# Kernel tuning notes

Measured on AMD Instinct MI355X. Metric: run time of the kernel, lower is better.

## Reference

```python
import jax, jax.numpy as jnp
import numpy as np

B, T, LMAX = 8, 4000, 2048
VOCAB, D, H = 20000, 128, 128
SCALE = float(H) ** 0.5  # torch uses pow(hidden_dim, 0.5) with hidden_dim=128 even though feature dim is 256


def setup_inputs() -> dict:
    key = jax.random.key(0)
    ks = jax.random.split(key, 22)
    def n(k, sh, s=0.05):
        return jax.random.normal(k, sh, dtype=jnp.float32) * s
    token_ids = jax.random.randint(ks[0], (B, T), 0, VOCAB)
    lens = jax.random.randint(ks[1], (B,), LMAX // 4, LMAX).at[0].set(LMAX)
    return dict(
        token_ids=token_ids, lens=lens,
        embed=n(ks[2], (VOCAB, D)),
        gru_wih0=n(ks[3], (2, 3 * H, D)), gru_whh0=n(ks[4], (2, 3 * H, H)),
        gru_bih0=n(ks[5], (2, 3 * H)), gru_bhh0=n(ks[6], (2, 3 * H)),
        gru_wih1=n(ks[7], (2, 3 * H, 2 * H)), gru_whh1=n(ks[8], (2, 3 * H, H)),
        gru_bih1=n(ks[9], (2, 3 * H)), gru_bhh1=n(ks[10], (2, 3 * H)),
        conv_w=n(ks[11], (3, D, D, 2)), conv_b=n(ks[12], (3, D)),
        Wa_w=n(ks[13], (2 * H, 4 * H)), Wa_b=n(ks[14], (2 * H,)),
        VT_w=n(ks[15], (1, 2 * H)), VT_b=n(ks[16], (1,)),
        Qw=n(ks[17], (2 * H, 2 * H)), Kw=n(ks[18], (2 * H, 2 * H)), Vw=n(ks[19], (2 * H, 2 * H)),
        fc_w=n(ks[20], (6, 2 * H)), fc_b=n(ks[21], (6,)),
    )


def _gru_dir(x, mask, Wih, Whh, bih, bhh):
    # One direction of a torch GRU layer with packed-sequence semantics:
    # outputs are zero past each sample's length; state frozen there.
    xg = jnp.einsum('bld,gd->blg', x, Wih) + bih   # [B, L, 3H] precomputed input gates
    xg = jnp.swapaxes(xg, 0, 1)                    # [L, B, 3H]
    m = jnp.swapaxes(mask, 0, 1)                   # [L, B]
    h0 = jnp.zeros((x.shape[0], H), x.dtype)

    def step(h, inp):
        g, mt = inp
        hh = h @ Whh.T + bhh
        r = jax.nn.sigmoid(g[:, :H] + hh[:, :H])
        z = jax.nn.sigmoid(g[:, H:2 * H] + hh[:, H:2 * H])
        nn_ = jnp.tanh(g[:, 2 * H:] + r * hh[:, 2 * H:])
        hn = (1.0 - z) * nn_ + z * h
        h2 = jnp.where(mt[:, None] > 0, hn, h)
        return h2, hn * mt[:, None]

    _, out = jax.lax.scan(step, h0, (xg, m))
    return jnp.swapaxes(out, 0, 1)                 # [B, L, H]


def _bi_gru_layer(x, mask, rev_idx, wih, whh, bih, bhh):
    out_f = _gru_dir(x, mask, wih[0], whh[0], bih[0], bhh[0])
    # packed bi-GRU: backward direction runs over each sample's reversed VALID segment
    xr = jnp.take_along_axis(x, rev_idx[:, :, None], axis=1)
    out_b = _gru_dir(xr, mask, wih[1], whh[1], bih[1], bhh[1])
    out_b = jnp.take_along_axis(out_b, rev_idx[:, :, None], axis=1) * mask[:, :, None]
    return jnp.concatenate([out_f, out_b], axis=-1)


def _additive_attn(s, enc, mask, Wa_w, Wa_b, VT_w, VT_b):
    sb = jnp.broadcast_to(s, enc.shape)
    x = jnp.concatenate([sb, enc], axis=-1)                     # [B, L, 4H]
    sh = jnp.tanh(jnp.einsum('blk,hk->blh', x, Wa_w) + Wa_b)
    res = jnp.einsum('blh,oh->blo', sh, VT_w)[..., 0] + VT_b[0]  # [B, L]
    # torch multiplies scores by 0/1 mask BEFORE softmax (pads get score 0, not -inf)
    w = jax.nn.softmax(res * mask, axis=-1)
    return jnp.sum(enc * w[..., None], axis=1, keepdims=True)   # [B, 1, 2H]


def _forward(embed, gru_wih0, gru_whh0, gru_bih0, gru_bhh0, gru_wih1, gru_whh1, gru_bih1, gru_bhh1,
             conv_w, conv_b, Wa_w, Wa_b, VT_w, VT_b, Qw, Kw, Vw, fc_w, fc_b, token_ids, lens):
    emb = embed[token_ids]                                      # [B, T, D]
    tpos = jnp.arange(LMAX)
    mask = (tpos[None, :] < lens[:, None]).astype(emb.dtype)    # [B, LMAX]
    rev_idx = jnp.where(tpos[None, :] < lens[:, None], lens[:, None] - 1 - tpos[None, :], tpos[None, :])
    pad_data = emb[:, :LMAX] * mask[..., None]                  # pad_packed_sequence zeroes pads

    # conv backbone runs on the FULL 4000-length padded embedding (as in torch), then trimmed/masked
    x = jnp.swapaxes(emb, 1, 2)                                 # [B, D, T]
    for i in range(3):
        x = jax.lax.conv_general_dilated(x, conv_w[i], (1,), 'VALID',
                                         dimension_numbers=('NCH', 'OIH', 'NCH'))
        x = jax.nn.relu(x + conv_b[i][None, :, None])
    conv_out = jnp.swapaxes(x, 1, 2)[:, :LMAX] * mask[..., None]  # [B, LMAX, D]

    h1 = _bi_gru_layer(pad_data, mask, rev_idx, gru_wih0, gru_whh0, gru_bih0, gru_bhh0)
    enc = _bi_gru_layer(h1, mask, rev_idx, gru_wih1, gru_whh1, gru_bih1, gru_bhh1)  # [B, LMAX, 2H]

    tmean = jnp.mean(conv_out, axis=1)                          # mean over padded length, as torch
    s = jnp.repeat(tmean, 2, axis=-1)[:, None, :]               # expand+reshape => interleaved duplicate [B,1,2H]

    inp2 = jnp.concatenate([pad_data, pad_data], axis=-1)       # [B, LMAX, 2H]
    Q = inp2 @ Qw.T
    K = inp2 @ Kw.T
    V = inp2 @ Vw.T
    scores = jnp.einsum('bqd,bkd->bqk', Q, K) / SCALE
    W = jax.nn.softmax(scores, axis=0)                          # torch F.softmax implicit dim -> 0 for 3D input
    W = W * mask[:, :, None]                                    # mask broadcast over key axis (query rows masked)
    Z = jnp.einsum('bqk,bkd->bqd', W, V)
    sa = jnp.sum(Z, axis=1, keepdims=True)                      # [B, 1, 2H]

    d1 = _additive_attn(s, enc, mask, Wa_w, Wa_b, VT_w, VT_b)
    d2 = _additive_attn(sa, enc, mask, Wa_w, Wa_b, VT_w, VT_b)
    dinput = 0.5 * (d1 + d2)                                    # mean over the concat dim
    return dinput @ fc_w.T + fc_b                               # [B, 1, 6]


def reference(token_ids, lens, embed, gru_wih0, gru_whh0, gru_bih0, gru_bhh0, gru_wih1, gru_whh1,
              gru_bih1, gru_bhh1, conv_w, conv_b, Wa_w, Wa_b, VT_w, VT_b, Qw, Kw, Vw, fc_w, fc_b):
    return _forward(embed, gru_wih0, gru_whh0, gru_bih0, gru_bhh0, gru_wih1, gru_whh1, gru_bih1,
                    gru_bhh1, conv_w, conv_b, Wa_w, Wa_b, VT_w, VT_b, Qw, Kw, Vw, fc_w, fc_b,
                    token_ids, lens)
```

## Files before the change

### kernel.cpp

```cpp
#include <hip/hip_runtime.h>
#include <stdint.h>

typedef unsigned short u16;
typedef unsigned int u32;
typedef __attribute__((ext_vector_type(8))) short short8;
typedef __attribute__((ext_vector_type(8))) u16 u16x8;
typedef __attribute__((ext_vector_type(4))) float f32x4;
typedef __attribute__((ext_vector_type(2))) float f32x2;
typedef __attribute__((ext_vector_type(2))) u32 u32x2;

#define DEVINL static __device__ __forceinline__

#if !__has_builtin(__builtin_amdgcn_exp2f)
#define __builtin_amdgcn_exp2f(x) exp2f(x)
#endif
#if !__has_builtin(__builtin_amdgcn_rcpf)
#define __builtin_amdgcn_rcpf(x) (1.0f/(x))
#endif

#define MFMA16(a, b, c) __builtin_amdgcn_mfma_f32_16x16x32_bf16((a), (b), (c), 0, 0, 0)

constexpr float LOG2E_C    = 1.4426950408889634f;
constexpr float TWOLOG2E_C = 2.8853900817779268f;
constexpr float RSCALE_LG  = 1.4426950408889634f / 11.313708498984761f;

constexpr size_t A256(size_t x){ return (x + 255) & ~(size_t)255; }
constexpr size_t OFS_EMB   = 0;
constexpr size_t OFS_PAD   = A256(OFS_EMB  + (size_t)8*2051*128*2);
constexpr size_t OFS_X1    = A256(OFS_PAD  + (size_t)8*2048*128*2);
constexpr size_t OFS_X2    = A256(OFS_X1   + (size_t)8*2050*128*2);
constexpr size_t OFS_QKVW  = A256(OFS_X2   + (size_t)8*2049*128*2);
constexpr size_t OFS_WA2   = A256(OFS_QKVW + (size_t)3*256*128*2);
constexpr size_t OFS_CONVW = A256(OFS_WA2  + (size_t)256*256*2);
constexpr size_t OFS_WIH0  = A256(OFS_CONVW+ (size_t)3*128*256*2);
constexpr size_t OFS_WIH1  = A256(OFS_WIH0 + (size_t)2*384*128*2);
constexpr size_t OFS_BIASX = A256(OFS_WIH1 + (size_t)2*384*256*2);
constexpr size_t OFS_BHHN  = A256(OFS_BIASX+ (size_t)2*2*384*4);
constexpr size_t OFS_Q     = A256(OFS_BHHN + (size_t)2*2*128*4);
constexpr size_t OFS_K     = A256(OFS_Q    + (size_t)8*2048*256*2);
constexpr size_t OFS_V     = A256(OFS_K    + (size_t)8*2048*256*2);
constexpr size_t OFS_CS    = A256(OFS_V    + (size_t)8*2048*256*2);
constexpr size_t OFS_TM    = A256(OFS_CS   + (size_t)8*2048*4);
constexpr size_t OFS_XG    = A256(OFS_TM   + (size_t)8*128*4);
constexpr size_t OFS_H1    = A256(OFS_XG   + (size_t)2*2048*8*384*4);
constexpr size_t OFS_ENC   = A256(OFS_H1   + (size_t)8*2048*256*2);
constexpr size_t OFS_ENCW  = A256(OFS_ENC  + (size_t)8*2048*256*2);
constexpr size_t OFS_SA    = A256(OFS_ENCW + (size_t)8*2048*256*4);
constexpr size_t OFS_RES   = A256(OFS_SA   + (size_t)8*256*4);
constexpr size_t OFS_DV    = A256(OFS_RES  + (size_t)8*2*2048*4);

DEVINL u16 f2bf(float f){
  u32 u = __builtin_bit_cast(u32, f);
  u32 r = (u + 0x7FFFu + ((u >> 16) & 1u)) >> 16;
  return (u16)r;
}
DEVINL float bf2f(u16 s){ return __builtin_bit_cast(float, (u32)s << 16); }

DEVINL short8 ld8cvt(const float* p, float sc){
  short8 o;
#pragma unroll
  for (int e = 0; e < 8; ++e) o[e] = (short)f2bf(p[e]*sc);
  return o;
}

DEVINL u32 cvtpk(float lo, float hi){
  u32 r;
  asm("v_cvt_pk_bf16_f32 %0, %1, %2" : "=v"(r) : "v"(lo), "v"(hi));
  return r;
}

DEVINL float sel4(const f32x4 v, int rr){
  float a = (rr & 1) ? v[1] : v[0];
  float bq = (rr & 1) ? v[3] : v[2];
  return (rr & 2) ? bq : a;
}

__global__ __launch_bounds__(256) void k_prep(
    const int* tok, const int* lens, const float* embed,
    const float* wih0, const float* wih1,
    const float* bih0, const float* bhh0, const float* bih1, const float* bhh1,
    const float* convw, const float* WaW, const float* Qw, const float* Kw, const float* Vw,
    char* ws)
{
  u16* emb_bf   = (u16*)(ws + OFS_EMB);
  u16* pad_bf   = (u16*)(ws + OFS_PAD);
  u16* qkvw     = (u16*)(ws + OFS_QKVW);
  u16* wa2      = (u16*)(ws + OFS_WA2);
  u16* convw_bf = (u16*)(ws + OFS_CONVW);
  u16* wih0_bf  = (u16*)(ws + OFS_WIH0);
  u16* wih1_bf  = (u16*)(ws + OFS_WIH1);
  float* biasx  = (float*)(ws + OFS_BIASX);
  float* bhhn   = (float*)(ws + OFS_BHHN);
  float* colsum = (float*)(ws + OFS_CS);
  float* tmean  = (float*)(ws + OFS_TM);
  const int S0 = 8*2051*128, S1 = 8*2048*128, S2 = 3*256*128, S3 = 256*256, S4 = 3*128*256;
  const int S5 = 2*384*128, S6 = 2*384*256, S7 = 2*2*384 + 2*2*128, S8 = 8*2048 + 8*128;
  const int TOT = S0+S1+S2+S3+S4+S5+S6+S7+S8;
  for (int i = blockIdx.x*256 + threadIdx.x; i < TOT; i += gridDim.x*256){
    int j = i;
    if (j < S0){
      int b = j / (2051*128); int r = j - b*(2051*128); int t = r >> 7, dd = r & 127;
      emb_bf[j] = f2bf(embed[(size_t)tok[b*4000 + t]*128 + dd]);
      continue;
    }
    j -= S0;
    if (j < S1){
      int b = j >> 18; int r = j & 262143; int t = r >> 7, dd = r & 127;
      float v = (t < lens[b]) ? embed[(size_t)tok[b*4000 + t]*128 + dd] : 0.f;
      pad_bf[j] = f2bf(v); continue;
    }
    j -= S1;
    if (j < S2){
      int z = j >> 15; int r = j & 32767; int o = r >> 7, k2 = r & 127;
      const float* W = (z == 0) ? Qw : (z == 1) ? Kw : Vw;
      qkvw[j] = f2bf(W[o*256 + k2] + W[o*256 + 128 + k2]); continue;
    }
    j -= S2;
    if (j < S3){ int h = j >> 8, k2 = j & 255; wa2[j] = f2bf(WaW[(size_t)h*512 + 256 + k2]); continue; }
    j -= S3;
    if (j < S4){
      int ly = j >> 15; int r = j & 32767; int o = r >> 8, k2 = r & 255;
      int i2 = k2 & 127, kap = k2 >> 7;
      convw_bf[j] = f2bf(convw[((size_t)(ly*128 + o)*128 + i2)*2 + kap]); continue;
    }
    j -= S4;
    if (j < S5){ wih0_bf[j] = f2bf(wih0[j]); continue; }
    j -= S5;
    if (j < S6){ wih1_bf[j] = f2bf(wih1[j]); continue; }
    j -= S6;
    if (j < S7){
      if (j < 1536){
        int ly = j / 768; int r = j - ly*768; int d = r / 384, g = r % 384;
        float bi = (ly ? bih1 : bih0)[d*384 + g];
        float bh = (ly ? bhh1 : bhh0)[d*384 + g];
        biasx[j] = (g < 256) ? (-LOG2E_C*(bi + bh)) : (TWOLOG2E_C*bi);
      } else {
        int j2 = j - 1536; int ly = j2 >> 8; int r = j2 & 255; int d = r >> 7, jj = r & 127;
        bhhn[j2] = TWOLOG2E_C*((ly ? bhh1 : bhh0)[d*384 + 256 + jj]);
      }
      continue;
    }
    j -= S7;
    if (j < 8*2048) colsum[j] = 0.f; else tmean[j - 8*2048] = 0.f;
  }
}

template<int LIN, int LOUT, int LAYER>
__global__ __launch_bounds__(256, 1) void k_conv(const int* lens, const float* convb, char* ws){
  const int tt = blockIdx.x, b = blockIdx.y;
  const u16* in = (LAYER == 0) ? (const u16*)(ws + OFS_EMB)
                : (LAYER == 1) ? (const u16*)(ws + OFS_X1) : (const u16*)(ws + OFS_X2);
  u16* out = (LAYER == 0) ? (u16*)(ws + OFS_X1) : (u16*)(ws + OFS_X2);
  const u16* wmat = (const u16*)(ws + OFS_CONVW) + (size_t)LAYER*128*256;
  float* tmean = (float*)(ws + OFS_TM);
  __shared__ __align__(16) u16 sA[65][136];
  const int tid = threadIdx.x, w = tid >> 6, l = tid & 63, rowg = l >> 4, cl = l & 15;
  for (int idx = tid; idx < 65*16; idx += 256){
    int row = idx >> 4, chn = idx & 15;
    int t = tt*64 + row;
    u16x8 v = {0,0,0,0,0,0,0,0};
    if (t < LIN) v = *(const u16x8*)(in + ((size_t)(b*LIN + t))*128 + chn*8);
    *(u16x8*)&sA[row][chn*8] = v;
  }
  __syncthreads();
  f32x4 acc[8];
#pragma unroll
  for (int nt = 0; nt < 8; ++nt) acc[nt] = f32x4{0.f,0.f,0.f,0.f};
#pragma unroll
  for (int kk = 0; kk < 8; ++kk){
    const int rofs = (kk >= 4) ? 1 : 0;
    short8 a = *(const short8*)&sA[w*16 + cl + rofs][(kk & 3)*32 + rowg*8];
#pragma unroll
    for (int nt = 0; nt < 8; ++nt){
      short8 bb = *(const short8*)(wmat + (size_t)(nt*16 + cl)*256 + kk*32 + rowg*8);
      acc[nt] = MFMA16(a, bb, acc[nt]);
    }
  }
  if (LAYER < 2){
#pragma unroll
    for (int nt = 0; nt < 8; ++nt){
      int o = nt*16 + cl;
      float bias = convb[LAYER*128 + o];
#pragma unroll
      for (int r = 0; r < 4; ++r){
        int t = tt*64 + w*16 + rowg*4 + r;
        if (t < LOUT) out[((size_t)(b*LOUT + t))*128 + o] = f2bf(fmaxf(acc[nt][r] + bias, 0.f));
      }
    }
  } else {
    const int lenb = lens[b];
#pragma unroll
    for (int nt = 0; nt < 8; ++nt){
      int o = nt*16 + cl;
      float bias = convb[2*128 + o];
      float s = 0.f;
#pragma unroll
      for (int r = 0; r < 4; ++r){
        int t = tt*64 + w*16 + rowg*4 + r;
        if (t < lenb) s += fmaxf(acc[nt][r] + bias, 0.f);
      }
      s += __shfl_xor(s, 16); s += __shfl_xor(s, 32);
      if (l < 16) atomicAdd(&tmean[b*128 + o], s);
    }
  }
}

__global__ __launch_bounds__(256, 1) void k_qkv(char* ws){
  const int tt = blockIdx.x, b = blockIdx.y, z = blockIdx.z;
  const u16* in = (const u16*)(ws + OFS_PAD);
  const u16* wmat = (const u16*)(ws + OFS_QKVW) + (size_t)z*256*128;
  u16* out = (u16*)(ws + ((z == 0) ? OFS_Q : (z == 1) ? OFS_K : OFS_V));
  __shared__ __align__(16) u16 sA[64][136];
  const int tid = threadIdx.x, w = tid >> 6, l = tid & 63, rowg = l >> 4, cl = l & 15;
  for (int idx = tid; idx < 64*16; idx += 256){
    int row = idx >> 4, chn = idx & 15;
    int t = tt*64 + row;
    *(u16x8*)&sA[row][chn*8] = *(const u16x8*)(in + ((size_t)(b*2048 + t))*128 + chn*8);
  }
  __syncthreads();
  f32x4 acc[16];
#pragma unroll
  for (int nt = 0; nt < 16; ++nt) acc[nt] = f32x4{0.f,0.f,0.f,0.f};
#pragma unroll
  for (int kk = 0; kk < 4; ++kk){
    short8 a = *(const short8*)&sA[w*16 + cl][kk*32 + rowg*8];
#pragma unroll
    for (int nt = 0; nt < 16; ++nt){
      short8 bb = *(const short8*)(wmat + (size_t)(nt*16 + cl)*128 + kk*32 + rowg*8);
      acc[nt] = MFMA16(a, bb, acc[nt]);
    }
  }
#pragma unroll
  for (int nt = 0; nt < 16; ++nt){
    int o = nt*16 + cl;
#pragma unroll
    for (int r = 0; r < 4; ++r){
      int t = tt*64 + w*16 + rowg*4 + r;
      out[((size_t)(b*2048 + t))*256 + o] = f2bf(acc[nt][r]);
    }
  }
}

__global__ __launch_bounds__(256, 1) void k_scores(const int* lens, char* ws){
  const int kt = blockIdx.x, qt = blockIdx.y;
  const u16* Qp = (const u16*)(ws + OFS_Q);
  const u16* Kp = (const u16*)(ws + OFS_K);
  float* colsum = (float*)(ws + OFS_CS);
  __shared__ __align__(16) u16 sQ[64][264];
  __shared__ __align__(16) u16 sK[64][264];
  __shared__ float cbuf[8][64];
  const int tid = threadIdx.x, w = tid >> 6, l = tid & 63, rowg = l >> 4, cl = l & 15;
  for (int i = tid; i < 512; i += 256) cbuf[i >> 6][i & 63] = 0.f;
  f32x4 c[8][4];
#pragma unroll
  for (int b = 0; b < 8; ++b)
#pragma unroll
    for (int nt = 0; nt < 4; ++nt) c[b][nt] = f32x4{0.f,0.f,0.f,0.f};
#pragma unroll
  for (int b = 0; b < 8; ++b){
    __syncthreads();
    for (int idx = tid; idx < 4096; idx += 256){
      int which = idx >> 11, row = (idx >> 5) & 63, ch = idx & 31;
      if (which){
        *(u16x8*)&sK[row][ch*8] = *(const u16x8*)(Kp + ((size_t)(b*2048 + kt*64 + row))*256 + ch*8);
      } else {
        *(u16x8*)&sQ[row][ch*8] = *(const u16x8*)(Qp + ((size_t)(b*2048 + qt*64 + row))*256 + ch*8);
      }
    }
    __syncthreads();
#pragma unroll
    for (int kk = 0; kk < 8; ++kk){
      short8 a = *(const short8*)&sQ[w*16 + cl][kk*32 + rowg*8];
#pragma unroll
      for (int nt = 0; nt < 4; ++nt){
        short8 bb = *(const short8*)&sK[nt*16 + cl][kk*32 + rowg*8];
        c[b][nt] = MFMA16(a, bb, c[b][nt]);
      }
    }
  }
  int lenv[8];
#pragma unroll
  for (int b = 0; b < 8; ++b) lenv[b] = lens[b];
  const int q0 = qt*64 + w*16 + rowg*4;
  float cs[8][4];
#pragma unroll
  for (int b = 0; b < 8; ++b)
#pragma unroll
    for (int nt = 0; nt < 4; ++nt) cs[b][nt] = 0.f;
#pragma unroll
  for (int nt = 0; nt < 4; ++nt){
#pragma unroll
    for (int r = 0; r < 4; ++r){
      float m = c[0][nt][r];
#pragma unroll
      for (int b = 1; b < 8; ++b) m = fmaxf(m, c[b][nt][r]);
      float e[8], s = 0.f;
#pragma unroll
      for (int b = 0; b < 8; ++b){ e[b] = __builtin_amdgcn_exp2f((c[b][nt][r] - m)*RSCALE_LG); s += e[b]; }
      float ri = __builtin_amdgcn_rcpf(s);
#pragma unroll
      for (int b = 0; b < 8; ++b)
        if (q0 + r < lenv[b]) cs[b][nt] += e[b]*ri;
    }
  }
#pragma unroll
  for (int b = 0; b < 8; ++b)
#pragma unroll
    for (int nt = 0; nt < 4; ++nt){
      float v = cs[b][nt];
      v += __shfl_xor(v, 16); v += __shfl_xor(v, 32);
      if (l < 16) atomicAdd(&cbuf[b][nt*16 + l], v);
    }
  __syncthreads();
  for (int i = tid; i < 512; i += 256)
    atomicAdd(&colsum[(size_t)(i >> 6)*2048 + kt*64 + (i & 63)], cbuf[i >> 6][i & 63]);
}

template<int KIN>
__global__ __launch_bounds__(256, 1) void k_xg(const int* lens, char* ws){
  const int tt = blockIdx.x, b = blockIdx.y, dir = blockIdx.z;
  constexpr int LAYER = (KIN == 128) ? 0 : 1;
  const u16* in = (KIN == 128) ? (const u16*)(ws + OFS_PAD) : (const u16*)(ws + OFS_H1);
  const u16* wmat = ((KIN == 128) ? (const u16*)(ws + OFS_WIH0) : (const u16*)(ws + OFS_WIH1))
                    + (size_t)dir*384*KIN;
  const float* biasx = (const float*)(ws + OFS_BIASX) + (LAYER*2 + dir)*384;
  float* xg = (float*)(ws + OFS_XG) + (size_t)dir*2048*3072;
  const int lenb = lens[b];
  __shared__ __align__(16) u16 sA[64][KIN + 8];
  constexpr int CH = KIN/8;
  const int tid = threadIdx.x, w = tid >> 6, l = tid & 63, rowg = l >> 4, cl = l & 15;
  for (int idx = tid; idx < 64*CH; idx += 256){
    int row = idx / CH, chn = idx % CH;
    int t = tt*64 + row;
    int tr = dir ? ((t < lenb) ? (lenb - 1 - t) : t) : t;
    *(u16x8*)&sA[row][chn*8] = *(const u16x8*)(in + ((size_t)(b*2048 + tr))*KIN + chn*8);
  }
  __syncthreads();
  f32x4 acc[24];
#pragma unroll
  for (int nt = 0; nt < 24; ++nt) acc[nt] = f32x4{0.f,0.f,0.f,0.f};
#pragma unroll
  for (int kk = 0; kk < KIN/32; ++kk){
    short8 a = *(const short8*)&sA[w*16 + cl][kk*32 + rowg*8];
#pragma unroll
    for (int nt = 0; nt < 24; ++nt){
      short8 bb = *(const short8*)(wmat + (size_t)(nt*16 + cl)*KIN + kk*32 + rowg*8);
      acc[nt] = MFMA16(a, bb, acc[nt]);
    }
  }
#pragma unroll
  for (int nt = 0; nt < 24; ++nt){
    const int g = nt*16 + cl;
    const float bx = biasx[g];
    const float sc = (nt < 16) ? -LOG2E_C : TWOLOG2E_C;
#pragma unroll
    for (int r = 0; r < 4; ++r){
      const int t = tt*64 + w*16 + rowg*4 + r;
      xg[((size_t)t*8 + b)*384 + g] = sc*acc[nt][r] + bx;
    }
  }
}

__global__ __launch_bounds__(512, 1) void k_rec(const float* xg_all, const float* whh_all,
    const float* bhhn_all, const int* lens, u16* out)
{
  const int dir = blockIdx.x >> 3;
  const int b   = blockIdx.x & 7;
  const float* xg  = xg_all + (size_t)dir*2048*3072 + b*384;
  const float* whh = whh_all + (size_t)dir*384*128;
  const float* bnd = bhhn_all + dir*128;
  const int tid = threadIdx.x;
  const int u = tid >> 6, l = tid & 63;
  const int c = l & 15, q = l >> 4;
  const int rsel = c & 3;
  const int j = u*16 + q*4 + rsel;
  const bool writer = (c < 4);
  const bool dirb = (dir != 0);
  const int lenb = lens[b];

  __shared__ __align__(16) u16 hbuf[2][128];
  if (tid < 256) (&hbuf[0][0])[tid] = 0;

  short8 aR[4], aZ[4], aN[4];
#pragma unroll
  for (int kk = 0; kk < 4; ++kk){
    int k0 = kk*32 + q*8;
    int row = u*16 + c;
    aR[kk] = ld8cvt(whh + (size_t)(row)*128 + k0, -LOG2E_C);
    aZ[kk] = ld8cvt(whh + (size_t)(128 + row)*128 + k0, -LOG2E_C);
    aN[kk] = ld8cvt(whh + (size_t)(256 + row)*128 + k0, TWOLOG2E_C);
  }
  f32x4 bnU;
#pragma unroll
  for (int r = 0; r < 4; ++r) bnU[r] = bnd[u*16 + q*4 + r];

  const int offR = u*16 + q*4;
  const int offXN = 256 + j;
  u16* outp = out + (size_t)b*2048*256 + dir*128 + j;
  float hp = 0.f;

#define LOAD_STAGE(T_, Rv, Zv, Xn) do {              \
    const float* pb_ = xg + (size_t)(T_)*3072;       \
    Rv = *(const f32x4*)(pb_ + offR);                \
    Zv = *(const f32x4*)(pb_ + offR + 128);          \
    Xn = pb_[offXN];                                 \
  } while (0)

#define REC_STEP(T_, PF_, CUR_, Rv, Zv, Xn) do {                                      \
    short8 bf0_ = *(const short8*)(&hbuf[CUR_][0] + (q*8 + 0*32));                    \
    short8 bf1_ = *(const short8*)(&hbuf[CUR_][0] + (q*8 + 1*32));                    \
    short8 bf2_ = *(const short8*)(&hbuf[CUR_][0] + (q*8 + 2*32));                    \
    short8 bf3_ = *(const short8*)(&hbuf[CUR_][0] + (q*8 + 3*32));                    \
    f32x4 cR_ = MFMA16(aR[0], bf0_, Rv);                                              \
    f32x4 cZ_ = MFMA16(aZ[0], bf0_, Zv);                                              \
    f32x4 cN_ = MFMA16(aN[0], bf0_, bnU);                                             \
    const float* pfb_ = xg + (size_t)(PF_)*3072;                                      \
    Rv = *(const f32x4*)(pfb_ + offR);                                                \
    Zv = *(const f32x4*)(pfb_ + offR + 128);                                          \
    float Xnew_ = pfb_[offXN];                                                        \
    cR_ = MFMA16(aR[1], bf1_, cR_);                                                   \
    cZ_ = MFMA16(aZ[1], bf1_, cZ_);                                                   \
    cN_ = MFMA16(aN[1], bf1_, cN_);                                                   \
    cR_ = MFMA16(aR[2], bf2_, cR_);                                                   \
    cZ_ = MFMA16(aZ[2], bf2_, cZ_);                                                   \
    cN_ = MFMA16(aN[2], bf2_, cN_);                                                   \
    cR_ = MFMA16(aR[3], bf3_, cR_);                                                   \
    cZ_ = MFMA16(aZ[3], bf3_, cZ_);                                                   \
    cN_ = MFMA16(aN[3], bf3_, cN_);                                                   \
    const bool v_ = (T_) < lenb;                                                      \
    float gR = sel4(cR_, rsel);                                                       \
    float gZ = sel4(cZ_, rsel);                                                       \
    float gN = sel4(cN_, rsel);                                                       \
    float Rg = __builtin_amdgcn_rcpf(1.f + __builtin_amdgcn_exp2f(gR));               \
    float Zg = __builtin_amdgcn_rcpf(1.f + __builtin_amdgcn_exp2f(gZ));               \
    float y  = Xn + Rg*gN;                                                            \
    float NN = 1.f - 2.f*__builtin_amdgcn_rcpf(1.f + __builtin_amdgcn_exp2f(y));      \
    float hn = NN + Zg*(hp - NN);                                                     \
    hp = hn;                                                                          \
    Xn = Xnew_;                                                                       \
    u32 pk_ = cvtpk(hn, hn);                                                          \
    if (writer){                                                                      \
      hbuf[(CUR_) ^ 1][j] = (u16)pk_;                                                 \
      int to_ = dirb ? (v_ ? (lenb - 1 - (T_)) : (T_)) : (T_);                        \
      outp[(size_t)to_*256] = v_ ? (u16)pk_ : (u16)0;                                 \
    }                                                                                 \
    asm volatile("s_waitcnt lgkmcnt(0)" ::: "memory");                                \
    __builtin_amdgcn_s_barrier();                                                     \
  } while (0)

  f32x4 R0v, Z0v; float X0;
  f32x4 R1v, Z1v; float X1;
  f32x4 R2v, Z2v; float X2;
  f32x4 R3v, Z3v; float X3;
  __syncthreads();
  LOAD_STAGE(0, R0v, Z0v, X0);
  LOAD_STAGE(1, R1v, Z1v, X1);
  LOAD_STAGE(2, R2v, Z2v, X2);
  LOAD_STAGE(3, R3v, Z3v, X3);
  for (int t = 0; t < 2048; t += 4){
    int p4 = (t + 4 < 2048) ? (t + 4) : 2047;
    int p5 = (t + 5 < 2048) ? (t + 5) : 2047;
    int p6 = (t + 6 < 2048) ? (t + 6) : 2047;
    int p7 = (t + 7 < 2048) ? (t + 7) : 2047;
    REC_STEP(t + 0, p4, 0, R0v, Z0v, X0);
    REC_STEP(t + 1, p5, 1, R1v, Z1v, X1);
    REC_STEP(t + 2, p6, 0, R2v, Z2v, X2);
    REC_STEP(t + 3, p7, 1, R3v, Z3v, X3);
  }
#undef LOAD_STAGE
#undef REC_STEP
}

__global__ __launch_bounds__(256, 1) void k_encw(char* ws){
  const int tt = blockIdx.x, b = blockIdx.y;
  const u16* in = (const u16*)(ws + OFS_ENC);
  const u16* wmat = (const u16*)(ws + OFS_WA2);
  float* out = (float*)(ws + OFS_ENCW);
  __shared__ __align__(16) u16 sA[64][264];
  const int tid = threadIdx.x, w = tid >> 6, l = tid & 63, rowg = l >> 4, cl = l & 15;
  for (int idx = tid; idx < 64*32; idx += 256){
    int row = idx >> 5, chn = idx & 31;
    int t = tt*64 + row;
    *(u16x8*)&sA[row][chn*8] = *(const u16x8*)(in + ((size_t)(b*2048 + t))*256 + chn*8);
  }
  __syncthreads();
  f32x4 acc[16];
#pragma unroll
  for (int nt = 0; nt < 16; ++nt) acc[nt] = f32x4{0.f,0.f,0.f,0.f};
#pragma unroll
  for (int kk = 0; kk < 8; ++kk){
    short8 a = *(const short8*)&sA[w*16 + cl][kk*32 + rowg*8];
#pragma unroll
    for (int nt = 0; nt < 16; ++nt){
      short8 bb = *(const short8*)(wmat + (size_t)(nt*16 + cl)*256 + kk*32 + rowg*8);
      acc[nt] = MFMA16(a, bb, acc[nt]);
    }
  }
#pragma unroll
  for (int nt = 0; nt < 16; ++nt){
    int h = nt*16 + cl;
#pragma unroll
    for (int r = 0; r < 4; ++r){
      int t = tt*64 + w*16 + rowg*4 + r;
      out[((size_t)(b*2048 + t))*256 + h] = acc[nt][r];
    }
  }
}

__global__ __launch_bounds__(256) void k_sa(char* ws){
  const int b = blockIdx.x, d = threadIdx.x;
  const float* cs = (const float*)(ws + OFS_CS) + (size_t)b*2048;
  const u16* V = (const u16*)(ws + OFS_V) + (size_t)b*2048*256;
  float a0 = 0.f, a1 = 0.f, a2 = 0.f, a3 = 0.f;
  for (int k = 0; k < 2048; k += 4){
    a0 += cs[k + 0]*bf2f(V[(size_t)(k + 0)*256 + d]);
    a1 += cs[k + 1]*bf2f(V[(size_t)(k + 1)*256 + d]);
    a2 += cs[k + 2]*bf2f(V[(size_t)(k + 2)*256 + d]);
    a3 += cs[k + 3]*bf2f(V[(size_t)(k + 3)*256 + d]);
  }
  ((float*)(ws + OFS_SA))[b*256 + d] = (a0 + a1) + (a2 + a3);
}

__global__ __launch_bounds__(256) void k_res(const int* lens, const float* WaW, const float* Wab,
    const float* VTw, const float* VTb, char* ws){
  const int b = blockIdx.x, x = blockIdx.y, chb = blockIdx.z;
  const float* tm = (const float*)(ws + OFS_TM) + b*128;
  const float* sa = (const float*)(ws + OFS_SA) + b*256;
  const float* encW = (const float*)(ws + OFS_ENCW);
  float* res = (float*)(ws + OFS_RES) + ((size_t)b*2 + x)*2048;
  __shared__ float sw[256];
  __shared__ float vt[256];
  const int tid = threadIdx.x;
  {
    int h = tid;
    float acc = Wab[h];
    if (x == 0){
      for (int j = 0; j < 128; ++j)
        acc += tm[j]*(1.f/2048.f)*(WaW[(size_t)h*512 + 2*j] + WaW[(size_t)h*512 + 2*j + 1]);
    } else {
      for (int k = 0; k < 256; ++k) acc += sa[k]*WaW[(size_t)h*512 + k];
    }
    sw[h] = acc;
    vt[h] = VTw[h];
  }
  __syncthreads();
  const int lenb = lens[b];
  const int lsub = tid >> 2, q = tid & 3;
  const float vtb = VTb[0];
#pragma unroll
  for (int pass = 0; pass < 4; ++pass){
    const int ll = chb*256 + pass*64 + lsub;
    const float* er = encW + ((size_t)(b*2048 + ll))*256 + q*64;
    float racc = 0.f;
    for (int j = 0; j < 64; ++j){
      float u = er[j] + sw[q*64 + j];
      float th = 1.f - 2.f*__builtin_amdgcn_rcpf(1.f + __builtin_amdgcn_exp2f(u*TWOLOG2E_C));
      racc += th*vt[q*64 + j];
    }
    racc += __shfl_xor(racc, 1);
    racc += __shfl_xor(racc, 2);
    if (q == 0) res[ll] = (ll < lenb) ? (racc + vtb) : 0.f;
  }
}

__global__ __launch_bounds__(256) void k_attnfin(char* ws){
  const int b = blockIdx.x, x = blockIdx.y;
  const float* res = (const float*)(ws + OFS_RES) + ((size_t)b*2 + x)*2048;
  const u16* enc = (const u16*)(ws + OFS_ENC);
  float* dvec = (float*)(ws + OFS_DV);
  __shared__ float sv[2048];
  __shared__ float red[8];
  const int tid = threadIdx.x;
  float m = -3.0e38f;
  for (int i = tid; i < 2048; i += 256){ float v = res[i]; sv[i] = v; m = fmaxf(m, v); }
#pragma unroll
  for (int o = 1; o < 64; o <<= 1) m = fmaxf(m, __shfl_xor(m, o));
  if ((tid & 63) == 0) red[tid >> 6] = m;
  __syncthreads();
  m = fmaxf(fmaxf(red[0], red[1]), fmaxf(red[2], red[3]));
  __syncthreads();
  float s = 0.f;
  for (int i = tid; i < 2048; i += 256){ float e = __builtin_amdgcn_exp2f((sv[i] - m)*LOG2E_C); sv[i] = e; s += e; }
#pragma unroll
  for (int o = 1; o < 64; o <<= 1) s += __shfl_xor(s, o);
  if ((tid & 63) == 0) red[tid >> 6] = s;
  __syncthreads();
  const float S = red[0] + red[1] + red[2] + red[3];
  const float ri = 1.0f/S;
  const int h = tid;
  float a0 = 0.f, a1 = 0.f, a2 = 0.f, a3 = 0.f;
  for (int l0 = 0; l0 < 2048; l0 += 4){
    a0 += sv[l0 + 0]*bf2f(enc[((size_t)(b*2048 + l0 + 0))*256 + h]);
    a1 += sv[l0 + 1]*bf2f(enc[((size_t)(b*2048 + l0 + 1))*256 + h]);
    a2 += sv[l0 + 2]*bf2f(enc[((size_t)(b*2048 + l0 + 2))*256 + h]);
    a3 += sv[l0 + 3]*bf2f(enc[((size_t)(b*2048 + l0 + 3))*256 + h]);
  }
  dvec[((size_t)b*2 + x)*256 + h] = ((a0 + a1) + (a2 + a3))*ri;
}

__global__ __launch_bounds__(64) void k_final(const float* fcw, const float* fcb, char* ws, float* outp){
  const int i = threadIdx.x;
  if (i >= 48) return;
  const int b = i/6, o = i%6;
  const float* dv = (const float*)(ws + OFS_DV);
  float acc = fcb[o];
  for (int h = 0; h < 256; ++h)
    acc += 0.5f*(dv[((size_t)b*2 + 0)*256 + h] + dv[((size_t)b*2 + 1)*256 + h])*fcw[o*256 + h];
  outp[i] = acc;
}

extern "C" void kernel_launch(void* const* d_in, const int* in_sizes, int n_in,
                              void* d_out, int out_size, void* d_ws, size_t ws_size,
                              hipStream_t stream)
{
  const int* tok    = (const int*)d_in[0];
  const int* lens   = (const int*)d_in[1];
  const float* embed= (const float*)d_in[2];
  const float* wih0 = (const float*)d_in[3];
  const float* whh0 = (const float*)d_in[4];
  const float* bih0 = (const float*)d_in[5];
  const float* bhh0 = (const float*)d_in[6];
  const float* wih1 = (const float*)d_in[7];
  const float* whh1 = (const float*)d_in[8];
  const float* bih1 = (const float*)d_in[9];
  const float* bhh1 = (const float*)d_in[10];
  const float* convw= (const float*)d_in[11];
  const float* convb= (const float*)d_in[12];
  const float* WaW  = (const float*)d_in[13];
  const float* Wab  = (const float*)d_in[14];
  const float* VTw  = (const float*)d_in[15];
  const float* VTb  = (const float*)d_in[16];
  const float* Qw   = (const float*)d_in[17];
  const float* Kw   = (const float*)d_in[18];
  const float* Vw   = (const float*)d_in[19];
  const float* fcw  = (const float*)d_in[20];
  const float* fcb  = (const float*)d_in[21];
  char* ws = (char*)d_ws;
  float* outp = (float*)d_out;

  hipLaunchKernelGGL(k_prep, dim3(2048), dim3(256), 0, stream,
      tok, lens, embed, wih0, wih1, bih0, bhh0, bih1, bhh1, convw, WaW, Qw, Kw, Vw, ws);
  hipLaunchKernelGGL((k_conv<2051,2050,0>), dim3(33,8), dim3(256), 0, stream, lens, convb, ws);
  hipLaunchKernelGGL((k_conv<2050,2049,1>), dim3(33,8), dim3(256), 0, stream, lens, convb, ws);
  hipLaunchKernelGGL((k_conv<2049,2048,2>), dim3(32,8), dim3(256), 0, stream, lens, convb, ws);
  hipLaunchKernelGGL(k_qkv, dim3(32,8,3), dim3(256), 0, stream, ws);
  hipLaunchKernelGGL(k_scores, dim3(32,32), dim3(256), 0, stream, lens, ws);
  hipLaunchKernelGGL((k_xg<128>), dim3(32,8,2), dim3(256), 0, stream, lens, ws);
  hipLaunchKernelGGL(k_rec, dim3(16), dim3(512), 0, stream,
      (const float*)(ws + OFS_XG), whh0, (const float*)(ws + OFS_BHHN), lens, (u16*)(ws + OFS_H1));
  hipLaunchKernelGGL((k_xg<256>), dim3(32,8,2), dim3(256), 0, stream, lens, ws);
  hipLaunchKernelGGL(k_rec, dim3(16), dim3(512), 0, stream,
      (const float*)(ws + OFS_XG), whh1, (const float*)(ws + OFS_BHHN) + 2*128, lens, (u16*)(ws + OFS_ENC));
  hipLaunchKernelGGL(k_encw, dim3(32,8), dim3(256), 0, stream, ws);
  hipLaunchKernelGGL(k_sa, dim3(8), dim3(256), 0, stream, ws);
  hipLaunchKernelGGL(k_res, dim3(8,2,8), dim3(256), 0, stream, lens, WaW, Wab, VTw, VTb, ws);
  hipLaunchKernelGGL(k_attnfin, dim3(8,2), dim3(256), 0, stream, ws);
  hipLaunchKernelGGL(k_final, dim3(1), dim3(64), 0, stream, fcw, fcb, ws, outp);
  (void)in_sizes; (void)n_in; (void)out_size; (void)ws_size;
}
```

Before: 1.981 ms.

## Overlap GRU recurrence with conv, QKV and scores work in fused role-split kernels

Merges the serial GRU recurrence blocks with independent parallel work (the conv stack and QKV projection in the first kernel, attention scores in the second) into role-dispatched launches. The otherwise idle CUs can then run that work while the 16 recurrence blocks run. The three conv layers are also fused into one per-tile pass that keeps intermediates in shared memory, recomputing halo rows. This risks the heavy roles contending with the latency-critical recurrence blocks for CU resources, adds a larger shared-memory footprint, and has half the threads idle in the non-recurrence roles.

```diff
diff --git a/kernel.cpp b/kernel.cpp
--- a/kernel.cpp
+++ b/kernel.cpp
@@ -145,177 +145,6 @@
   }
 }
 
-template<int LIN, int LOUT, int LAYER>
-__global__ __launch_bounds__(256, 1) void k_conv(const int* lens, const float* convb, char* ws){
-  const int tt = blockIdx.x, b = blockIdx.y;
-  const u16* in = (LAYER == 0) ? (const u16*)(ws + OFS_EMB)
-                : (LAYER == 1) ? (const u16*)(ws + OFS_X1) : (const u16*)(ws + OFS_X2);
-  u16* out = (LAYER == 0) ? (u16*)(ws + OFS_X1) : (u16*)(ws + OFS_X2);
-  const u16* wmat = (const u16*)(ws + OFS_CONVW) + (size_t)LAYER*128*256;
-  float* tmean = (float*)(ws + OFS_TM);
-  __shared__ __align__(16) u16 sA[65][136];
-  const int tid = threadIdx.x, w = tid >> 6, l = tid & 63, rowg = l >> 4, cl = l & 15;
-  for (int idx = tid; idx < 65*16; idx += 256){
-    int row = idx >> 4, chn = idx & 15;
-    int t = tt*64 + row;
-    u16x8 v = {0,0,0,0,0,0,0,0};
-    if (t < LIN) v = *(const u16x8*)(in + ((size_t)(b*LIN + t))*128 + chn*8);
-    *(u16x8*)&sA[row][chn*8] = v;
-  }
-  __syncthreads();
-  f32x4 acc[8];
-#pragma unroll
-  for (int nt = 0; nt < 8; ++nt) acc[nt] = f32x4{0.f,0.f,0.f,0.f};
-#pragma unroll
-  for (int kk = 0; kk < 8; ++kk){
-    const int rofs = (kk >= 4) ? 1 : 0;
-    short8 a = *(const short8*)&sA[w*16 + cl + rofs][(kk & 3)*32 + rowg*8];
-#pragma unroll
-    for (int nt = 0; nt < 8; ++nt){
-      short8 bb = *(const short8*)(wmat + (size_t)(nt*16 + cl)*256 + kk*32 + rowg*8);
-      acc[nt] = MFMA16(a, bb, acc[nt]);
-    }
-  }
-  if (LAYER < 2){
-#pragma unroll
-    for (int nt = 0; nt < 8; ++nt){
-      int o = nt*16 + cl;
-      float bias = convb[LAYER*128 + o];
-#pragma unroll
-      for (int r = 0; r < 4; ++r){
-        int t = tt*64 + w*16 + rowg*4 + r;
-        if (t < LOUT) out[((size_t)(b*LOUT + t))*128 + o] = f2bf(fmaxf(acc[nt][r] + bias, 0.f));
-      }
-    }
-  } else {
-    const int lenb = lens[b];
-#pragma unroll
-    for (int nt = 0; nt < 8; ++nt){
-      int o = nt*16 + cl;
-      float bias = convb[2*128 + o];
-      float s = 0.f;
-#pragma unroll
-      for (int r = 0; r < 4; ++r){
-        int t = tt*64 + w*16 + rowg*4 + r;
-        if (t < lenb) s += fmaxf(acc[nt][r] + bias, 0.f);
-      }
-      s += __shfl_xor(s, 16); s += __shfl_xor(s, 32);
-      if (l < 16) atomicAdd(&tmean[b*128 + o], s);
-    }
-  }
-}
-
-__global__ __launch_bounds__(256, 1) void k_qkv(char* ws){
-  const int tt = blockIdx.x, b = blockIdx.y, z = blockIdx.z;
-  const u16* in = (const u16*)(ws + OFS_PAD);
-  const u16* wmat = (const u16*)(ws + OFS_QKVW) + (size_t)z*256*128;
-  u16* out = (u16*)(ws + ((z == 0) ? OFS_Q : (z == 1) ? OFS_K : OFS_V));
-  __shared__ __align__(16) u16 sA[64][136];
-  const int tid = threadIdx.x, w = tid >> 6, l = tid & 63, rowg = l >> 4, cl = l & 15;
-  for (int idx = tid; idx < 64*16; idx += 256){
-    int row = idx >> 4, chn = idx & 15;
-    int t = tt*64 + row;
-    *(u16x8*)&sA[row][chn*8] = *(const u16x8*)(in + ((size_t)(b*2048 + t))*128 + chn*8);
-  }
-  __syncthreads();
-  f32x4 acc[16];
-#pragma unroll
-  for (int nt = 0; nt < 16; ++nt) acc[nt] = f32x4{0.f,0.f,0.f,0.f};
-#pragma unroll
-  for (int kk = 0; kk < 4; ++kk){
-    short8 a = *(const short8*)&sA[w*16 + cl][kk*32 + rowg*8];
-#pragma unroll
-    for (int nt = 0; nt < 16; ++nt){
-      short8 bb = *(const short8*)(wmat + (size_t)(nt*16 + cl)*128 + kk*32 + rowg*8);
-      acc[nt] = MFMA16(a, bb, acc[nt]);
-    }
-  }
-#pragma unroll
-  for (int nt = 0; nt < 16; ++nt){
-    int o = nt*16 + cl;
-#pragma unroll
-    for (int r = 0; r < 4; ++r){
-      int t = tt*64 + w*16 + rowg*4 + r;
-      out[((size_t)(b*2048 + t))*256 + o] = f2bf(acc[nt][r]);
-    }
-  }
-}
-
-__global__ __launch_bounds__(256, 1) void k_scores(const int* lens, char* ws){
-  const int kt = blockIdx.x, qt = blockIdx.y;
-  const u16* Qp = (const u16*)(ws + OFS_Q);
-  const u16* Kp = (const u16*)(ws + OFS_K);
-  float* colsum = (float*)(ws + OFS_CS);
-  __shared__ __align__(16) u16 sQ[64][264];
-  __shared__ __align__(16) u16 sK[64][264];
-  __shared__ float cbuf[8][64];
-  const int tid = threadIdx.x, w = tid >> 6, l = tid & 63, rowg = l >> 4, cl = l & 15;
-  for (int i = tid; i < 512; i += 256) cbuf[i >> 6][i & 63] = 0.f;
-  f32x4 c[8][4];
-#pragma unroll
-  for (int b = 0; b < 8; ++b)
-#pragma unroll
-    for (int nt = 0; nt < 4; ++nt) c[b][nt] = f32x4{0.f,0.f,0.f,0.f};
-#pragma unroll
-  for (int b = 0; b < 8; ++b){
-    __syncthreads();
-    for (int idx = tid; idx < 4096; idx += 256){
-      int which = idx >> 11, row = (idx >> 5) & 63, ch = idx & 31;
-      if (which){
-        *(u16x8*)&sK[row][ch*8] = *(const u16x8*)(Kp + ((size_t)(b*2048 + kt*64 + row))*256 + ch*8);
-      } else {
-        *(u16x8*)&sQ[row][ch*8] = *(const u16x8*)(Qp + ((size_t)(b*2048 + qt*64 + row))*256 + ch*8);
-      }
-    }
-    __syncthreads();
-#pragma unroll
-    for (int kk = 0; kk < 8; ++kk){
-      short8 a = *(const short8*)&sQ[w*16 + cl][kk*32 + rowg*8];
-#pragma unroll
-      for (int nt = 0; nt < 4; ++nt){
-        short8 bb = *(const short8*)&sK[nt*16 + cl][kk*32 + rowg*8];
-        c[b][nt] = MFMA16(a, bb, c[b][nt]);
-      }
-    }
-  }
-  int lenv[8];
-#pragma unroll
-  for (int b = 0; b < 8; ++b) lenv[b] = lens[b];
-  const int q0 = qt*64 + w*16 + rowg*4;
-  float cs[8][4];
-#pragma unroll
-  for (int b = 0; b < 8; ++b)
-#pragma unroll
-    for (int nt = 0; nt < 4; ++nt) cs[b][nt] = 0.f;
-#pragma unroll
-  for (int nt = 0; nt < 4; ++nt){
-#pragma unroll
-    for (int r = 0; r < 4; ++r){
-      float m = c[0][nt][r];
-#pragma unroll
-      for (int b = 1; b < 8; ++b) m = fmaxf(m, c[b][nt][r]);
-      float e[8], s = 0.f;
-#pragma unroll
-      for (int b = 0; b < 8; ++b){ e[b] = __builtin_amdgcn_exp2f((c[b][nt][r] - m)*RSCALE_LG); s += e[b]; }
-      float ri = __builtin_amdgcn_rcpf(s);
-#pragma unroll
-      for (int b = 0; b < 8; ++b)
-        if (q0 + r < lenv[b]) cs[b][nt] += e[b]*ri;
-    }
-  }
-#pragma unroll
-  for (int b = 0; b < 8; ++b)
-#pragma unroll
-    for (int nt = 0; nt < 4; ++nt){
-      float v = cs[b][nt];
-      v += __shfl_xor(v, 16); v += __shfl_xor(v, 32);
-      if (l < 16) atomicAdd(&cbuf[b][nt*16 + l], v);
-    }
-  __syncthreads();
-  for (int i = tid; i < 512; i += 256)
-    atomicAdd(&colsum[(size_t)(i >> 6)*2048 + kt*64 + (i & 63)], cbuf[i >> 6][i & 63]);
-}
-
 template<int KIN>
 __global__ __launch_bounds__(256, 1) void k_xg(const int* lens, char* ws){
   const int tt = blockIdx.x, b = blockIdx.y, dir = blockIdx.z;
@@ -361,11 +190,9 @@
   }
 }
 
-__global__ __launch_bounds__(512, 1) void k_rec(const float* xg_all, const float* whh_all,
-    const float* bhhn_all, const int* lens, u16* out)
+DEVINL void rec_block(char* smem, const float* xg_all, const float* whh_all,
+    const float* bhhn_all, const int* lens, u16* out, int dir, int b)
 {
-  const int dir = blockIdx.x >> 3;
-  const int b   = blockIdx.x & 7;
   const float* xg  = xg_all + (size_t)dir*2048*3072 + b*384;
   const float* whh = whh_all + (size_t)dir*384*128;
   const float* bnd = bhhn_all + dir*128;
@@ -378,7 +205,7 @@
   const bool dirb = (dir != 0);
   const int lenb = lens[b];
 
-  __shared__ __align__(16) u16 hbuf[2][128];
+  u16 (*hbuf)[128] = (u16(*)[128])smem;
   if (tid < 256) (&hbuf[0][0])[tid] = 0;
 
   short8 aR[4], aZ[4], aN[4];
@@ -471,6 +298,246 @@
 #undef REC_STEP
 }
 
+DEVINL void qkv_role(char* smem, char* ws, int tt, int b, int z){
+  const u16* in = (const u16*)(ws + OFS_PAD);
+  const u16* wmat = (const u16*)(ws + OFS_QKVW) + (size_t)z*256*128;
+  u16* out = (u16*)(ws + ((z == 0) ? OFS_Q : (z == 1) ? OFS_K : OFS_V));
+  u16 (*sA)[136] = (u16(*)[136])smem;
+  const int tid = threadIdx.x;
+  if (tid < 256){
+    for (int idx = tid; idx < 64*16; idx += 256){
+      int row = idx >> 4, chn = idx & 15;
+      int t = tt*64 + row;
+      *(u16x8*)&sA[row][chn*8] = *(const u16x8*)(in + ((size_t)(b*2048 + t))*128 + chn*8);
+    }
+  }
+  __syncthreads();
+  if (tid < 256){
+    const int w = tid >> 6, l = tid & 63, rowg = l >> 4, cl = l & 15;
+    f32x4 acc[16];
+#pragma unroll
+    for (int nt = 0; nt < 16; ++nt) acc[nt] = f32x4{0.f,0.f,0.f,0.f};
+#pragma unroll
+    for (int kk = 0; kk < 4; ++kk){
+      short8 a = *(const short8*)&sA[w*16 + cl][kk*32 + rowg*8];
+#pragma unroll
+      for (int nt = 0; nt < 16; ++nt){
+        short8 bb = *(const short8*)(wmat + (size_t)(nt*16 + cl)*128 + kk*32 + rowg*8);
+        acc[nt] = MFMA16(a, bb, acc[nt]);
+      }
+    }
+#pragma unroll
+    for (int nt = 0; nt < 16; ++nt){
+      int o = nt*16 + cl;
+#pragma unroll
+      for (int r = 0; r < 4; ++r){
+        int t = tt*64 + w*16 + rowg*4 + r;
+        out[((size_t)(b*2048 + t))*256 + o] = f2bf(acc[nt][r]);
+      }
+    }
+  }
+}
+
+DEVINL void conv_layer_pass(u16 (*bi)[136], u16 (*bo)[136], const u16* wm, const float* bias,
+                            int OUT_R, int w, int rowg, int cl){
+#pragma unroll
+  for (int pass = 0; pass < 2; ++pass){
+    if (pass == 1 && !(w == 0 && OUT_R > 64)) break;
+    const int rt = (pass == 0) ? w : 4;
+    f32x4 acc[8];
+#pragma unroll
+    for (int nt = 0; nt < 8; ++nt) acc[nt] = f32x4{0.f,0.f,0.f,0.f};
+#pragma unroll
+    for (int kk = 0; kk < 8; ++kk){
+      const int rofs = (kk >= 4) ? 1 : 0;
+      short8 a = *(const short8*)&bi[rt*16 + cl + rofs][(kk & 3)*32 + rowg*8];
+#pragma unroll
+      for (int nt = 0; nt < 8; ++nt){
+        short8 bb = *(const short8*)(wm + (size_t)(nt*16 + cl)*256 + kk*32 + rowg*8);
+        acc[nt] = MFMA16(a, bb, acc[nt]);
+      }
+    }
+#pragma unroll
+    for (int nt = 0; nt < 8; ++nt){
+      int o = nt*16 + cl;
+      float bv = bias[o];
+#pragma unroll
+      for (int r = 0; r < 4; ++r){
+        int ro = rt*16 + rowg*4 + r;
+        if (ro < OUT_R) bo[ro][o] = f2bf(fmaxf(acc[nt][r] + bv, 0.f));
+      }
+    }
+  }
+}
+
+DEVINL void conv_role(char* smem, const int* lens, const float* convb, char* ws, int tt, int b){
+  const u16* emb = (const u16*)(ws + OFS_EMB);
+  const u16* cw  = (const u16*)(ws + OFS_CONVW);
+  float* tmean = (float*)(ws + OFS_TM);
+  u16 (*bufA)[136] = (u16(*)[136])smem;
+  u16 (*bufB)[136] = (u16(*)[136])(smem + 82*136*2);
+  const int tid = threadIdx.x;
+  const int w = tid >> 6, l = tid & 63, rowg = l >> 4, cl = l & 15;
+  if (tid < 256){
+    for (int idx = tid; idx < 67*16; idx += 256){
+      int row = idx >> 4, chn = idx & 15;
+      *(u16x8*)&bufA[row][chn*8] = *(const u16x8*)(emb + ((size_t)(b*2051 + tt*64 + row))*128 + chn*8);
+    }
+  }
+  __syncthreads();
+  if (tid < 256) conv_layer_pass(bufA, bufB, cw + (size_t)0*128*256, convb + 0,   66, w, rowg, cl);
+  __syncthreads();
+  if (tid < 256) conv_layer_pass(bufB, bufA, cw + (size_t)1*128*256, convb + 128, 65, w, rowg, cl);
+  __syncthreads();
+  if (tid < 256){
+    const int lenb = lens[b];
+    const u16* wm = cw + (size_t)2*128*256;
+    f32x4 acc[8];
+#pragma unroll
+    for (int nt = 0; nt < 8; ++nt) acc[nt] = f32x4{0.f,0.f,0.f,0.f};
+#pragma unroll
+    for (int kk = 0; kk < 8; ++kk){
+      const int rofs = (kk >= 4) ? 1 : 0;
+      short8 a = *(const short8*)&bufA[w*16 + cl + rofs][(kk & 3)*32 + rowg*8];
+#pragma unroll
+      for (int nt = 0; nt < 8; ++nt){
+        short8 bb = *(const short8*)(wm + (size_t)(nt*16 + cl)*256 + kk*32 + rowg*8);
+        acc[nt] = MFMA16(a, bb, acc[nt]);
+      }
+    }
+#pragma unroll
+    for (int nt = 0; nt < 8; ++nt){
+      int o = nt*16 + cl;
+      float bias = convb[2*128 + o];
+      float s = 0.f;
+#pragma unroll
+      for (int r = 0; r < 4; ++r){
+        int t = tt*64 + w*16 + rowg*4 + r;
+        if (t < lenb) s += fmaxf(acc[nt][r] + bias, 0.f);
+      }
+      s += __shfl_xor(s, 16); s += __shfl_xor(s, 32);
+      if (l < 16) atomicAdd(&tmean[b*128 + o], s);
+    }
+  }
+}
+
+DEVINL void scores_role(char* smem, const int* lens, char* ws, int kt, int qt){
+  const u16* Qp = (const u16*)(ws + OFS_Q);
+  const u16* Kp = (const u16*)(ws + OFS_K);
+  float* colsum = (float*)(ws + OFS_CS);
+  u16 (*sQ)[264] = (u16(*)[264])smem;
+  u16 (*sK)[264] = (u16(*)[264])(smem + 64*264*2);
+  float (*cbuf)[64] = (float(*)[64])(smem + 2*64*264*2);
+  const int tid = threadIdx.x, w = tid >> 6, l = tid & 63, rowg = l >> 4, cl = l & 15;
+  if (tid < 256)
+    for (int i = tid; i < 512; i += 256) cbuf[i >> 6][i & 63] = 0.f;
+  f32x4 c[8][4];
+#pragma unroll
+  for (int b = 0; b < 8; ++b)
+#pragma unroll
+    for (int nt = 0; nt < 4; ++nt) c[b][nt] = f32x4{0.f,0.f,0.f,0.f};
+#pragma unroll
+  for (int b = 0; b < 8; ++b){
+    __syncthreads();
+    if (tid < 256){
+      for (int idx = tid; idx < 4096; idx += 256){
+        int which = idx >> 11, row = (idx >> 5) & 63, ch = idx & 31;
+        if (which){
+          *(u16x8*)&sK[row][ch*8] = *(const u16x8*)(Kp + ((size_t)(b*2048 + kt*64 + row))*256 + ch*8);
+        } else {
+          *(u16x8*)&sQ[row][ch*8] = *(const u16x8*)(Qp + ((size_t)(b*2048 + qt*64 + row))*256 + ch*8);
+        }
+      }
+    }
+    __syncthreads();
+    if (tid < 256){
+#pragma unroll
+      for (int kk = 0; kk < 8; ++kk){
+        short8 a = *(const short8*)&sQ[w*16 + cl][kk*32 + rowg*8];
+#pragma unroll
+        for (int nt = 0; nt < 4; ++nt){
+          short8 bb = *(const short8*)&sK[nt*16 + cl][kk*32 + rowg*8];
+          c[b][nt] = MFMA16(a, bb, c[b][nt]);
+        }
+      }
+    }
+  }
+  if (tid < 256){
+    int lenv[8];
+#pragma unroll
+    for (int b = 0; b < 8; ++b) lenv[b] = lens[b];
+    const int q0 = qt*64 + w*16 + rowg*4;
+    float cs[8][4];
+#pragma unroll
+    for (int b = 0; b < 8; ++b)
+#pragma unroll
+      for (int nt = 0; nt < 4; ++nt) cs[b][nt] = 0.f;
+#pragma unroll
+    for (int nt = 0; nt < 4; ++nt){
+#pragma unroll
+      for (int r = 0; r < 4; ++r){
+        float m = c[0][nt][r];
+#pragma unroll
+        for (int b = 1; b < 8; ++b) m = fmaxf(m, c[b][nt][r]);
+        float e[8], s = 0.f;
+#pragma unroll
+        for (int b = 0; b < 8; ++b){ e[b] = __builtin_amdgcn_exp2f((c[b][nt][r] - m)*RSCALE_LG); s += e[b]; }
+        float ri = __builtin_amdgcn_rcpf(s);
+#pragma unroll
+        for (int b = 0; b < 8; ++b)
+          if (q0 + r < lenv[b]) cs[b][nt] += e[b]*ri;
+      }
+    }
+#pragma unroll
+    for (int b = 0; b < 8; ++b)
+#pragma unroll
+      for (int nt = 0; nt < 4; ++nt){
+        float v = cs[b][nt];
+        v += __shfl_xor(v, 16); v += __shfl_xor(v, 32);
+        if (l < 16) atomicAdd(&cbuf[b][nt*16 + l], v);
+      }
+  }
+  __syncthreads();
+  if (tid < 256){
+    for (int i = tid; i < 512; i += 256)
+      atomicAdd(&colsum[(size_t)(i >> 6)*2048 + kt*64 + (i & 63)], cbuf[i >> 6][i & 63]);
+  }
+}
+
+__global__ __launch_bounds__(512, 2) void k_fusedA(const int* lens, const float* convb, char* ws,
+    const float* whh0, u16* outH1)
+{
+  __shared__ __align__(16) char smem[90112];
+  const int bid = blockIdx.x;
+  if (bid < 16){
+    rec_block(smem, (const float*)(ws + OFS_XG), whh0, (const float*)(ws + OFS_BHHN),
+              lens, outH1, bid >> 3, bid & 7);
+    return;
+  }
+  int r = bid - 16;
+  if (r < 768){
+    int z = r >> 8, rem = r & 255, b = rem >> 5, tt = rem & 31;
+    qkv_role(smem, ws, tt, b, z);
+    return;
+  }
+  r -= 768;
+  conv_role(smem, lens, convb, ws, r & 31, r >> 5);
+}
+
+__global__ __launch_bounds__(512, 2) void k_fusedB(const int* lens, char* ws,
+    const float* whh1, u16* outENC)
+{
+  __shared__ __align__(16) char smem[90112];
+  const int bid = blockIdx.x;
+  if (bid < 16){
+    rec_block(smem, (const float*)(ws + OFS_XG), whh1, (const float*)(ws + OFS_BHHN) + 2*128,
+              lens, outENC, bid >> 3, bid & 7);
+    return;
+  }
+  int r = bid - 16;
+  scores_role(smem, lens, ws, r & 31, r >> 5);
+}
+
 __global__ __launch_bounds__(256, 1) void k_encw(char* ws){
   const int tt = blockIdx.x, b = blockIdx.y;
   const u16* in = (const u16*)(ws + OFS_ENC);
@@ -640,19 +707,14 @@
 
   hipLaunchKernelGGL(k_prep, dim3(2048), dim3(256), 0, stream,
       tok, lens, embed, wih0, wih1, bih0, bhh0, bih1, bhh1, convw, WaW, Qw, Kw, Vw, ws);
-  hipLaunchKernelGGL((k_conv<2051,2050,0>), dim3(33,8), dim3(256), 0, stream, lens, convb, ws);
-  hipLaunchKernelGGL((k_conv<2050,2049,1>), dim3(33,8), dim3(256), 0, stream, lens, convb, ws);
-  hipLaunchKernelGGL((k_conv<2049,2048,2>), dim3(32,8), dim3(256), 0, stream, lens, convb, ws);
-  hipLaunchKernelGGL(k_qkv, dim3(32,8,3), dim3(256), 0, stream, ws);
-  hipLaunchKernelGGL(k_scores, dim3(32,32), dim3(256), 0, stream, lens, ws);
   hipLaunchKernelGGL((k_xg<128>), dim3(32,8,2), dim3(256), 0, stream, lens, ws);
-  hipLaunchKernelGGL(k_rec, dim3(16), dim3(512), 0, stream,
-      (const float*)(ws + OFS_XG), whh0, (const float*)(ws + OFS_BHHN), lens, (u16*)(ws + OFS_H1));
+  hipLaunchKernelGGL(k_fusedA, dim3(16 + 768 + 256), dim3(512), 0, stream,
+      lens, convb, ws, whh0, (u16*)(ws + OFS_H1));
   hipLaunchKernelGGL((k_xg<256>), dim3(32,8,2), dim3(256), 0, stream, lens, ws);
-  hipLaunchKernelGGL(k_rec, dim3(16), dim3(512), 0, stream,
-      (const float*)(ws + OFS_XG), whh1, (const float*)(ws + OFS_BHHN) + 2*128, lens, (u16*)(ws + OFS_ENC));
+  hipLaunchKernelGGL(k_fusedB, dim3(16 + 1024), dim3(512), 0, stream,
+      lens, ws, whh1, (u16*)(ws + OFS_ENC));
+  hipLaunchKernelGGL(k_sa, dim3(8), dim3(256), 0, stream, ws);
   hipLaunchKernelGGL(k_encw, dim3(32,8), dim3(256), 0, stream, ws);
-  hipLaunchKernelGGL(k_sa, dim3(8), dim3(256), 0, stream, ws);
   hipLaunchKernelGGL(k_res, dim3(8,2,8), dim3(256), 0, stream, lens, WaW, Wab, VTw, VTb, ws);
   hipLaunchKernelGGL(k_attnfin, dim3(8,2), dim3(256), 0, stream, ws);
   hipLaunchKernelGGL(k_final, dim3(1), dim3(64), 0, stream, fcw, fcb, ws, outp);
```

Result: faster. 1.799 ms (-9.2%).
